# Optimization experiments

Hardware: AMD Instinct MI355X
Metric: run time of the kernel (lower is better)

Reference implementation:

```python
import jax, jax.numpy as jnp
import numpy as np

B = 4             # graphs per batch
POS_RANGE = 240.0 # pos lives in [0, 240)^3
VOXELS = (20.0, 30.0, 50.0, 80.0)
NEG = -1e30


def _basis(u):
    # open B-spline basis, degree 1, kernel_size 2, dim 3 -> 8 weights per edge
    cols = []
    for k in range(8):
        w = (u[:, 0] if k & 4 else 1.0 - u[:, 0])
        w = w * (u[:, 1] if k & 2 else 1.0 - u[:, 1])
        w = w * (u[:, 2] if k & 1 else 1.0 - u[:, 2])
        cols.append(w)
    return jnp.stack(cols, axis=1)  # [E, 8]


def _cartesian(pos, src, dst, emask):
    # T.Cartesian(cat=False, norm=True): rel pos scaled into [0,1]
    rel = pos[src] - pos[dst]
    m = jnp.max(jnp.where(emask[:, None], jnp.abs(rel), 0.0))
    return rel / (2.0 * jnp.maximum(m, 1e-9)) + 0.5


def _spline_conv(x, src, dst, pseudo, emask, W, Wr, b, n_nodes):
    # out_i = mean_{j->i} sum_k B_k(u_ij) x_j W_k + x_i Wr + b
    basis = _basis(pseudo) * emask[:, None].astype(x.dtype)  # [E,8]
    xk = jnp.einsum('ni,kio->nko', x, W)                     # [N,8,O]
    msg = basis[:, 0, None] * xk[src, 0]
    for k in range(1, 8):
        msg = msg + basis[:, k, None] * xk[src, k]           # [E,O]
    agg = jax.ops.segment_sum(msg, dst, num_segments=n_nodes)
    deg = jax.ops.segment_sum(emask.astype(x.dtype), dst, num_segments=n_nodes)
    return agg / jnp.maximum(deg, 1.0)[:, None] + x @ Wr + b


def _voxel_ids(pos, batch, vs):
    G = int(np.ceil(POS_RANGE / vs))
    c = jnp.clip(jnp.floor(pos / vs).astype(jnp.int64), 0, G - 1)
    cell = (c[:, 0] * G + c[:, 1]) * G + c[:, 2]
    return batch * (G ** 3) + cell, G ** 3


def _max_pool(x, pos, batch, valid, src, dst, emask, vs):
    # voxel-grid max pooling: nodes become fixed voxel cells (empty cells masked)
    nid, ncells = _voxel_ids(pos, batch, vs)
    n_new = B * ncells
    xm = jnp.where(valid[:, None], x, NEG)
    x_p = jax.ops.segment_max(xm, nid, num_segments=n_new)
    cnt = jax.ops.segment_sum(valid.astype(x.dtype), nid, num_segments=n_new)
    v_new = cnt > 0
    x_p = jnp.where(v_new[:, None], x_p, 0.0)
    pos_p = jax.ops.segment_sum(pos * valid[:, None].astype(pos.dtype), nid, num_segments=n_new)
    pos_p = pos_p / jnp.maximum(cnt, 1.0)[:, None]
    batch_p = jnp.arange(n_new, dtype=jnp.int64) // ncells
    # coarsen edges: remap to cells, drop self loops, coalesce at fixed size
    s2, d2 = nid[src], nid[dst]
    sent = n_new * n_new
    key = jnp.where(emask & (s2 != d2), s2 * n_new + d2, sent)
    uk = jnp.unique(key, size=key.shape[0], fill_value=sent)
    em = uk != sent
    uk = jnp.where(em, uk, 0)
    return x_p, pos_p, batch_p, v_new, uk // n_new, uk % n_new, em


def setup_inputs():
    key = jax.random.key(0)
    ks = jax.random.split(key, 24)
    NP, DEG = 5000, 8
    N = B * NP
    E = N * DEG
    x = jax.random.normal(ks[0], (N, 1), dtype=jnp.float32)
    pos = jax.random.uniform(ks[1], (N, 3), dtype=jnp.float32) * POS_RANGE
    src = jnp.repeat(jnp.arange(N, dtype=jnp.int64), DEG)
    delta = jax.random.randint(ks[2], (E,), 1, 100, dtype=jnp.int64)
    dst = (src // NP) * NP + (src % NP + delta) % NP   # intra-graph edges
    edge_index = jnp.stack([src, dst])
    batch = jnp.arange(N, dtype=jnp.int64) // NP
    sizes = [1, 64, 128, 256, 512]
    params = {}
    for l in range(4):
        ci, co = sizes[l], sizes[l + 1]
        params[f'W{l+1}'] = jax.random.normal(ks[3 + 3 * l], (8, ci, co), dtype=jnp.float32) / np.sqrt(8.0 * ci)
        params[f'Wr{l+1}'] = jax.random.normal(ks[4 + 3 * l], (ci, co), dtype=jnp.float32) / np.sqrt(float(ci))
        params[f'b{l+1}'] = jnp.zeros((co,), dtype=jnp.float32)
    params['fc1_w'] = jax.random.normal(ks[16], (64 * 512, 1024), dtype=jnp.float32) / np.sqrt(64.0 * 512.0)
    params['fc1_b'] = jnp.zeros((1024,), dtype=jnp.float32)
    params['fc2_w'] = jax.random.normal(ks[17], (1024, 1), dtype=jnp.float32) / np.sqrt(1024.0)
    params['fc2_b'] = jnp.zeros((1,), dtype=jnp.float32)
    return dict(x=x, pos=pos, edge_index=edge_index, batch=batch, **params)


def reference(x, pos, edge_index, batch, W1, Wr1, b1, W2, Wr2, b2, W3, Wr3, b3,
              W4, Wr4, b4, fc1_w, fc1_b, fc2_w, fc2_b):
    src, dst = edge_index[0], edge_index[1]
    n_nodes = x.shape[0]
    valid = jnp.ones((n_nodes,), dtype=bool)
    emask = jnp.ones((src.shape[0],), dtype=bool)
    Ws = [(W1, Wr1, b1), (W2, Wr2, b2), (W3, Wr3, b3), (W4, Wr4, b4)]
    for l in range(4):
        pseudo = _cartesian(pos, src, dst, emask)
        W, Wr, b = Ws[l]
        x = jax.nn.elu(_spline_conv(x, src, dst, pseudo, emask, W, Wr, b, n_nodes))
        if l < 3:
            x, pos, batch, valid, src, dst, emask = _max_pool(x, pos, batch, valid, src, dst, emask, VOXELS[l])
            n_nodes = x.shape[0]
    # MaxPoolingX(voxel=80, size=64): ceil(240/80)^3 = 27 <= 64 slots per graph
    nid, ncells = _voxel_ids(pos, batch, VOXELS[3])
    cluster = batch * 64 + (nid % ncells)
    xm = jnp.where(valid[:, None], x, NEG)
    xg = jax.ops.segment_max(xm, cluster, num_segments=B * 64)
    xg = jnp.where(xg <= NEG / 2, 0.0, xg)      # empty slots -> 0 (scatter-max default)
    xg = xg.reshape(B, 64 * 512)
    h = jax.nn.elu(xg @ fc1_w + fc1_b)           # dropout = identity (eval mode)
    return jax.nn.elu(h @ fc2_w + fc2_b)         # [B, 1]
```

## Files before the change

### kernel.cpp

```cpp
#include <hip/hip_runtime.h>

static constexpr int E0 = 160000;
static constexpr int NL0 = 20000;
static constexpr int NL1 = 6912;
static constexpr int NL2 = 2048;
static constexpr int NL3 = 500;

typedef short bf16x8 __attribute__((ext_vector_type(8)));
typedef float f32x4 __attribute__((ext_vector_type(4)));

__device__ __forceinline__ unsigned f2ord(float f) {
  unsigned u = __float_as_uint(f);
  return (u & 0x80000000u) ? ~u : (u | 0x80000000u);
}
__device__ __forceinline__ float ord2f(unsigned u) {
  unsigned v = (u & 0x80000000u) ? (u & 0x7fffffffu) : ~u;
  return __uint_as_float(v);
}
__device__ __forceinline__ float eluf(float x) { return x > 0.f ? x : expm1f(x); }
__device__ __forceinline__ void basis8(float u0, float u1, float u2, float* w) {
  float a0 = 1.f - u0, a1 = 1.f - u1, a2 = 1.f - u2;
  w[0] = a0*a1*a2; w[1] = a0*a1*u2; w[2] = a0*u1*a2; w[3] = a0*u1*u2;
  w[4] = u0*a1*a2; w[5] = u0*a1*u2; w[6] = u0*u1*a2; w[7] = u0*u1*u2;
}
__device__ __forceinline__ unsigned short f2b(float f) {
  unsigned u = __float_as_uint(f);
  return (unsigned short)((u + 0x7fffu + ((u >> 16) & 1u)) >> 16);
}
__device__ __forceinline__ float b2f(unsigned short h) {
  return __uint_as_float(((unsigned)h) << 16);
}
__device__ __forceinline__ int clampi(int v, int lo, int hi) {
  return v < lo ? lo : (v > hi ? hi : v);
}

__device__ __forceinline__ void mfma_tile(const unsigned short* __restrict__ Ah,
    const unsigned short* __restrict__ Al, const unsigned short* __restrict__ Bh,
    const unsigned short* __restrict__ Bl, int M, long K, int m0, int n0,
    int kbeg, int ksl, char* smem, f32x4* acc) {
  auto Ash = (unsigned short (*)[40])(smem);
  auto Asl = (unsigned short (*)[40])(smem + 5120);
  auto Bsh = (unsigned short (*)[40])(smem + 10240);
  auto Bsl = (unsigned short (*)[40])(smem + 15360);
  int t = threadIdx.x;
  int r = t >> 2, sg = (t & 3) * 8;
  int w = t >> 6, lane = t & 63;
  int ar = (w << 4) + (lane & 15), kq = (lane >> 4) << 3;
  for (int kt = 0; kt < ksl; kt += 32) {
    bf16x8 va = {}, vl = {};
    if (m0 + r < M) {
      long ga = (long)(m0 + r) * K + kbeg + kt + sg;
      va = *(const bf16x8*)&Ah[ga];
      vl = *(const bf16x8*)&Al[ga];
    }
    *(bf16x8*)&Ash[r][sg] = va;
    *(bf16x8*)&Asl[r][sg] = vl;
    long gb = (long)(n0 + r) * K + kbeg + kt + sg;
    *(bf16x8*)&Bsh[r][sg] = *(const bf16x8*)&Bh[gb];
    *(bf16x8*)&Bsl[r][sg] = *(const bf16x8*)&Bl[gb];
    __syncthreads();
    bf16x8 ah = *(const bf16x8*)&Ash[ar][kq];
    bf16x8 al = *(const bf16x8*)&Asl[ar][kq];
    #pragma unroll
    for (int nt = 0; nt < 4; nt++) {
      int br = (nt << 4) + (lane & 15);
      bf16x8 bh = *(const bf16x8*)&Bsh[br][kq];
      bf16x8 bl = *(const bf16x8*)&Bsl[br][kq];
      acc[nt] = __builtin_amdgcn_mfma_f32_16x16x32_bf16(al, bh, acc[nt], 0, 0, 0);
      acc[nt] = __builtin_amdgcn_mfma_f32_16x16x32_bf16(ah, bl, acc[nt], 0, 0, 0);
      acc[nt] = __builtin_amdgcn_mfma_f32_16x16x32_bf16(ah, bh, acc[nt], 0, 0, 0);
    }
    __syncthreads();
  }
}

__global__ __launch_bounds__(256)
void k_prep(const int* __restrict__ src0, const int* __restrict__ dst0,
            const float* __restrict__ pos0, const float* __restrict__ x0,
            int* __restrict__ degi, int4* __restrict__ erec0u, float* __restrict__ mbuf,
            unsigned* __restrict__ zA, long zAw,
            const float* __restrict__ W1, const float* __restrict__ Wr1, float* __restrict__ wc1,
            const float* __restrict__ W2, const float* __restrict__ Wr2,
            const float* __restrict__ W3, const float* __restrict__ Wr3,
            const float* __restrict__ W4, const float* __restrict__ Wr4,
            unsigned short* __restrict__ w2h, unsigned short* __restrict__ w2l,
            unsigned short* __restrict__ w3h, unsigned short* __restrict__ w3l,
            unsigned short* __restrict__ w4h, unsigned short* __restrict__ w4l) {
  __shared__ __align__(16) float T[64][65];
  __shared__ float red[4];
  int tid = blockIdx.x * 256 + threadIdx.x;
  long gsz = (long)gridDim.x * 256;
  for (long i = tid; i < zAw; i += gsz) zA[i] = 0u;
  float v = 0.f;
  for (int e = tid; e < E0; e += (int)gsz) {
    int s = src0[e], d = dst0[e];
    atomicAdd(&degi[d], 1);
    float r0 = pos0[s*3]   - pos0[d*3];
    float r1 = pos0[s*3+1] - pos0[d*3+1];
    float r2 = pos0[s*3+2] - pos0[d*3+2];
    erec0u[e] = make_int4(__float_as_int(x0[s]), __float_as_int(r0),
                          __float_as_int(r1), __float_as_int(r2));
    v = fmaxf(v, fmaxf(fabsf(r0), fmaxf(fabsf(r1), fabsf(r2))));
  }
  #pragma unroll
  for (int off = 32; off; off >>= 1) v = fmaxf(v, __shfl_down(v, off, 64));
  if ((threadIdx.x & 63) == 0) red[threadIdx.x >> 6] = v;
  __syncthreads();
  if (threadIdx.x == 0)
    atomicMax((unsigned*)mbuf,
              __float_as_uint(fmaxf(fmaxf(red[0], red[1]), fmaxf(red[2], red[3]))));
  for (int b = blockIdx.x; b < 378; b += gridDim.x) {
    const float *W, *Wr; unsigned short *oh, *ol; int K, N, kt, nt;
    if (b < 18)      { W = W2; Wr = Wr2; oh = w2h; ol = w2l; K = 576;  N = 128; kt = b / 2; nt = b % 2; }
    else if (b < 90) { int q = b - 18; W = W3; Wr = Wr3; oh = w3h; ol = w3l; K = 1152; N = 256; kt = q / 4; nt = q % 4; }
    else             { int q = b - 90; W = W4; Wr = Wr4; oh = w4h; ol = w4l; K = 2304; N = 512; kt = q / 8; nt = q % 8; }
    int k0 = kt * 64, n0 = nt * 64, KW = K - K / 9;
    __syncthreads();
    for (int i = threadIdx.x; i < 4096; i += 256) {
      int kk = i >> 6, nn = i & 63, k = k0 + kk;
      T[kk][nn] = (k < KW) ? W[(long)k * N + n0 + nn] : Wr[(long)(k - KW) * N + n0 + nn];
    }
    __syncthreads();
    for (int i = threadIdx.x; i < 4096; i += 256) {
      int nn = i >> 6, kk = i & 63;
      float vv = T[kk][nn];
      unsigned short hu = f2b(vv), lu = f2b(vv - b2f(hu));
      long o = (long)(n0 + nn) * K + k0 + kk;
      oh[o] = hu; ol[o] = lu;
    }
  }
  if (blockIdx.x == 0)
    for (int i = threadIdx.x; i < 576; i += 256)
      wc1[i] = (i < 512) ? W1[i] : Wr1[i - 512];
}

__global__ void k_alloc(int* __restrict__ degi, int* __restrict__ rowbeg,
                        int* __restrict__ rowlen, int* __restrict__ cursor,
                        int* __restrict__ ctr, int N) {
  int n = blockIdx.x * 256 + threadIdx.x;
  if (n >= N) return;
  int len = degi[n];
  int st = atomicAdd(ctr, len);
  rowbeg[n] = st; cursor[n] = st; rowlen[n] = len; degi[n] = 0;
}

__global__ void k_scat(const int4* __restrict__ eu, const int* __restrict__ du,
                       const int* __restrict__ ecnt, int ecap,
                       int* __restrict__ cursor, int4* __restrict__ es) {
  int n = ecnt ? *ecnt : ecap;
  for (int e = blockIdx.x * 256 + threadIdx.x; e < n; e += gridDim.x * 256) {
    int p = atomicAdd(&cursor[du[e]], 1);
    es[p] = eu[e];
  }
}

__global__ __launch_bounds__(256)
void k_l1(const int4* __restrict__ erec, const int* __restrict__ rowbeg,
          const int* __restrict__ rowlen, const float* __restrict__ mbuf,
          const float* __restrict__ x0, const float* __restrict__ pos0,
          const float* __restrict__ wc1, const float* __restrict__ b1,
          unsigned* __restrict__ pord1, float* __restrict__ cnt1,
          float* __restrict__ possum1, int* __restrict__ nid) {
  __shared__ float wls[576];
  __shared__ float b1s[64];
  __shared__ float ys[32][12];
  int t = threadIdx.x;
  for (int i = t; i < 576; i += 256) wls[i] = wc1[i];
  if (t < 64) b1s[t] = b1[t];
  int d = blockIdx.x * 32 + (t >> 3);
  int sub = t & 7;
  float inv = 0.5f / fmaxf(mbuf[0], 1e-9f);
  if (d < NL0) {
    int beg = rowbeg[d], len = rowlen[d], end = beg + len;
    float acc[8] = {};
    for (int j = beg + sub; j < end; j += 8) {
      int4 rc = erec[j];
      float xv = __int_as_float(rc.x);
      float w[8];
      basis8(__int_as_float(rc.y) * inv + 0.5f, __int_as_float(rc.z) * inv + 0.5f,
             __int_as_float(rc.w) * inv + 0.5f, w);
      #pragma unroll
      for (int k = 0; k < 8; k++) acc[k] += w[k] * xv;
    }
    #pragma unroll
    for (int m = 1; m < 8; m <<= 1)
      #pragma unroll
      for (int k = 0; k < 8; k++) acc[k] += __shfl_xor(acc[k], m, 64);
    if (sub == 0) {
      float sc = 1.f / fmaxf((float)len, 1.f);
      int nl = t >> 3;
      #pragma unroll
      for (int k = 0; k < 8; k++) ys[nl][k] = acc[k] * sc;
      ys[nl][8]  = x0[d];
      ys[nl][9]  = pos0[d*3];
      ys[nl][10] = pos0[d*3+1];
      ys[nl][11] = pos0[d*3+2];
    }
  }
  __syncthreads();
  #pragma unroll 2
  for (int it = 0; it < 8; it++) {
    int idx = it * 256 + t;
    int nl = idx >> 6, ch = idx & 63;
    int dd = blockIdx.x * 32 + nl;
    if (dd < NL0) {
      float v = b1s[ch] + ys[nl][8] * wls[512 + ch];
      #pragma unroll
      for (int k = 0; k < 8; k++) v += ys[nl][k] * wls[k * 64 + ch];
      v = eluf(v);
      float pd0 = ys[nl][9], pd1 = ys[nl][10], pd2 = ys[nl][11];
      int c0 = clampi((int)floorf(pd0 / 20.f), 0, 11);
      int c1 = clampi((int)floorf(pd1 / 20.f), 0, 11);
      int c2 = clampi((int)floorf(pd2 / 20.f), 0, 11);
      int id = (dd / 5000) * 1728 + (c0 * 12 + c1) * 12 + c2;
      atomicMax(&pord1[(long)id * 64 + ch], f2ord(v));
      if (ch == 0) {
        nid[dd] = id;
        atomicAdd(&cnt1[id], 1.f);
        atomicAdd(&possum1[id*3],   pd0);
        atomicAdd(&possum1[id*3+1], pd1);
        atomicAdd(&possum1[id*3+2], pd2);
      }
    }
  }
}

__global__ __launch_bounds__(256)
void k_pedge(const int4* __restrict__ erecf, const int* __restrict__ srcf,
             const int* __restrict__ dstf, const int* __restrict__ ecntf, int ecap,
             const int* __restrict__ nid, int Nn, unsigned* __restrict__ bitmap,
             int4* __restrict__ erecu, int* __restrict__ dstu, int* __restrict__ ecntc,
             int* __restrict__ degi, const float* __restrict__ possum,
             const float* __restrict__ cnt, float* __restrict__ mo) {
  __shared__ float red[4];
  int n = ecntf ? *ecntf : ecap;
  int lane = threadIdx.x & 63;
  int stride = gridDim.x * 256;
  float vmax = 0.f;
  for (int base = blockIdx.x * 256; base < n; base += stride) {
    int e = base + threadIdx.x;
    bool win = false;
    int s2 = 0, d2 = 0;
    float r0 = 0.f, r1 = 0.f, r2 = 0.f;
    if (e < n) {
      int sL = erecf ? erecf[e].x : srcf[e];
      int dL = dstf[e];
      s2 = nid[sL]; d2 = nid[dL];
      if (s2 != d2) {
        float ics = 1.f / fmaxf(cnt[s2], 1.f), icd = 1.f / fmaxf(cnt[d2], 1.f);
        r0 = possum[s2*3]   * ics - possum[d2*3]   * icd;
        r1 = possum[s2*3+1] * ics - possum[d2*3+1] * icd;
        r2 = possum[s2*3+2] * ics - possum[d2*3+2] * icd;
        vmax = fmaxf(vmax, fmaxf(fabsf(r0), fmaxf(fabsf(r1), fabsf(r2))));
        unsigned key = (unsigned)s2 * (unsigned)Nn + (unsigned)d2;
        unsigned bit = 1u << (key & 31);
        unsigned old = atomicOr(&bitmap[key >> 5], bit);
        win = !(old & bit);
      }
    }
    unsigned long long mask = __ballot(win);
    if (mask) {
      int leader = __ffsll((unsigned long long)mask) - 1;
      int bq = 0;
      if (lane == leader) bq = atomicAdd(ecntc, __popcll(mask));
      bq = __shfl(bq, leader, 64);
      if (win) {
        int q = bq + __popcll(mask & ((1ULL << lane) - 1ULL));
        erecu[q] = make_int4(s2, __float_as_int(r0), __float_as_int(r1), __float_as_int(r2));
        dstu[q] = d2;
        atomicAdd(&degi[d2], 1);
      }
    }
  }
  #pragma unroll
  for (int off = 32; off; off >>= 1) vmax = fmaxf(vmax, __shfl_down(vmax, off, 64));
  if ((threadIdx.x & 63) == 0) red[threadIdx.x >> 6] = vmax;
  __syncthreads();
  if (threadIdx.x == 0)
    atomicMax((unsigned*)mo,
              __float_as_uint(fmaxf(fmaxf(red[0], red[1]), fmaxf(red[2], red[3]))));
}

template<int ES>
__global__ __launch_bounds__(256)
void k_gather(const unsigned* __restrict__ pordc, const int4* __restrict__ erec,
              const int* __restrict__ rowbeg, const int* __restrict__ rowlen,
              const float* __restrict__ mbuf,
              unsigned short* __restrict__ ysh, unsigned short* __restrict__ ysl,
              int N, int Ci, int nchunk,
              unsigned* __restrict__ zp, long zw) {
  for (long i = (long)blockIdx.x * 256 + threadIdx.x; i < zw;
       i += (long)gridDim.x * 256) zp[i] = 0u;
  __shared__ float comb[4][64][8];
  int wv = threadIdx.x >> 6, lane = threadIdx.x & 63;
  int gw = blockIdx.x * 4 + wv;
  int job = gw / ES, sub = gw % ES;
  int d = job / nchunk, ch = job % nchunk;
  bool active = d < N;
  float inv = 0.5f / fmaxf(mbuf[0], 1e-9f);
  int co = ch * 64 + lane;
  float acc[8] = {};
  int beg = 0, len = 0;
  if (active) {
    beg = rowbeg[d]; len = rowlen[d];
    int end = beg + len;
    int j = beg + sub;
    for (; j + 3 * ES < end; j += 4 * ES) {
      int4 ra = erec[j], rb = erec[j + ES], rc = erec[j + 2 * ES], rd = erec[j + 3 * ES];
      float xa = ord2f(pordc[(long)ra.x * Ci + co]);
      float xb = ord2f(pordc[(long)rb.x * Ci + co]);
      float xc = ord2f(pordc[(long)rc.x * Ci + co]);
      float xd = ord2f(pordc[(long)rd.x * Ci + co]);
      float wa[8], wb[8], wc[8], wd[8];
      basis8(__int_as_float(ra.y) * inv + 0.5f, __int_as_float(ra.z) * inv + 0.5f,
             __int_as_float(ra.w) * inv + 0.5f, wa);
      basis8(__int_as_float(rb.y) * inv + 0.5f, __int_as_float(rb.z) * inv + 0.5f,
             __int_as_float(rb.w) * inv + 0.5f, wb);
      basis8(__int_as_float(rc.y) * inv + 0.5f, __int_as_float(rc.z) * inv + 0.5f,
             __int_as_float(rc.w) * inv + 0.5f, wc);
      basis8(__int_as_float(rd.y) * inv + 0.5f, __int_as_float(rd.z) * inv + 0.5f,
             __int_as_float(rd.w) * inv + 0.5f, wd);
      #pragma unroll
      for (int k = 0; k < 8; k++)
        acc[k] += wa[k] * xa + wb[k] * xb + wc[k] * xc + wd[k] * xd;
    }
    for (; j < end; j += ES) {
      int4 ra = erec[j];
      float xa = ord2f(pordc[(long)ra.x * Ci + co]);
      float wa[8];
      basis8(__int_as_float(ra.y) * inv + 0.5f, __int_as_float(ra.z) * inv + 0.5f,
             __int_as_float(ra.w) * inv + 0.5f, wa);
      #pragma unroll
      for (int k = 0; k < 8; k++) acc[k] += wa[k] * xa;
    }
  }
  if (ES > 1) {
    #pragma unroll
    for (int k = 0; k < 8; k++) comb[wv][lane][k] = acc[k];
    __syncthreads();
    if (sub != 0 || !active) return;
    #pragma unroll
    for (int s = 1; s < ES; s++)
      #pragma unroll
      for (int k = 0; k < 8; k++) acc[k] += comb[wv + s][lane][k];
  } else if (!active) return;
  float sc = 1.f / fmaxf((float)len, 1.f);
  long row = (long)d * 9 * Ci;
  #pragma unroll
  for (int k = 0; k < 8; k++) {
    float v = acc[k] * sc;
    unsigned short hu = f2b(v);
    ysh[row + k * Ci + co] = hu;
    ysl[row + k * Ci + co] = f2b(v - b2f(hu));
  }
  unsigned od = pordc[(long)d * Ci + co];
  float xdv = (od == 0u) ? 0.f : ord2f(od);
  unsigned short hu = f2b(xdv);
  ysh[row + 8 * Ci + co] = hu;
  ysl[row + 8 * Ci + co] = f2b(xdv - b2f(hu));
}

__global__ __launch_bounds__(256)
void k_gemmpool(const unsigned short* __restrict__ ysh, const unsigned short* __restrict__ ysl,
                const unsigned short* __restrict__ Bh, const unsigned short* __restrict__ Bl,
                int M, int N, int K, const float* __restrict__ bias,
                const float* __restrict__ possum, const float* __restrict__ cnt,
                int div, float vs, int G, int NC,
                unsigned* __restrict__ pordn, float* __restrict__ cntn,
                float* __restrict__ possumn, int* __restrict__ nid) {
  __shared__ __align__(16) char smem[20480];
  int nbx = N >> 6;
  int bx = blockIdx.x % nbx, by = blockIdx.x / nbx;
  int m0 = by * 64, n0 = bx * 64;
  f32x4 acc[4] = {};
  mfma_tile(ysh, ysl, Bh, Bl, M, K, m0, n0, 0, K, smem, acc);
  int w = threadIdx.x >> 6, lane = threadIdx.x & 63;
  int row0 = m0 + (w << 4) + ((lane >> 4) << 2);
  int colb = n0 + (lane & 15);
  #pragma unroll
  for (int q = 0; q < 4; q++) {
    int gm = row0 + q;
    float c = cnt[gm];
    float ic = 1.f / fmaxf(c, 1.f);
    float p0 = possum[gm*3] * ic, p1 = possum[gm*3+1] * ic, p2 = possum[gm*3+2] * ic;
    int c0 = clampi((int)floorf(p0 / vs), 0, G - 1);
    int c1 = clampi((int)floorf(p1 / vs), 0, G - 1);
    int c2 = clampi((int)floorf(p2 / vs), 0, G - 1);
    int id = (gm / div) * NC + (c0 * G + c1) * G + c2;
    bool vl = c > 0.f;
    if (bx == 0 && (lane & 15) == 0) {
      nid[gm] = id;
      if (vl) {
        atomicAdd(&cntn[id], 1.f);
        atomicAdd(&possumn[id*3],   p0);
        atomicAdd(&possumn[id*3+1], p1);
        atomicAdd(&possumn[id*3+2], p2);
      }
    }
    if (vl) {
      #pragma unroll
      for (int nt = 0; nt < 4; nt++) {
        int col = colb + nt * 16;
        float v = eluf(acc[nt][q] + bias[col]);
        atomicMax(&pordn[(long)id * N + col], f2ord(v));
      }
    }
  }
}

__global__ __launch_bounds__(256)
void k_gemm4(const unsigned short* __restrict__ ysh, const unsigned short* __restrict__ ysl,
             const unsigned short* __restrict__ Bh, const unsigned short* __restrict__ Bl,
             float* __restrict__ Cp, int* __restrict__ done,
             const float* __restrict__ b4, const float* __restrict__ possum3,
             const float* __restrict__ cnt3, unsigned* __restrict__ xg) {
  __shared__ __align__(16) char smem[20480];
  __shared__ int flag;
  int z = blockIdx.x >> 6, rem = blockIdx.x & 63, bx = rem & 7, by = rem >> 3;
  int m0 = by * 64, n0 = bx * 64;
  f32x4 acc[4] = {};
  mfma_tile(ysh, ysl, Bh, Bl, 500, 2304, m0, n0, z * 576, 576, smem, acc);
  float* Co = Cp + (long)z * 256000;
  int w = threadIdx.x >> 6, lane = threadIdx.x & 63;
  int row0 = m0 + (w << 4) + ((lane >> 4) << 2);
  int colb = n0 + (lane & 15);
  #pragma unroll
  for (int nt = 0; nt < 4; nt++)
    #pragma unroll
    for (int q = 0; q < 4; q++) {
      int gm = row0 + q;
      if (gm < 500) Co[(long)gm * 512 + colb + nt * 16] = acc[nt][q];
    }
  __threadfence();
  if (threadIdx.x == 0) flag = atomicAdd(&done[rem], 1);
  __syncthreads();
  if (flag != 3) return;
  __threadfence();
  #pragma unroll
  for (int q = 0; q < 4; q++) {
    int gm = row0 + q;
    if (gm >= 500) continue;
    float c = cnt3[gm];
    if (c <= 0.f) continue;
    float ic = 1.f / c;
    float p0 = possum3[gm*3] * ic, p1 = possum3[gm*3+1] * ic, p2 = possum3[gm*3+2] * ic;
    int c0 = clampi((int)floorf(p0 / 80.f), 0, 2);
    int c1 = clampi((int)floorf(p1 / 80.f), 0, 2);
    int c2 = clampi((int)floorf(p2 / 80.f), 0, 2);
    int cl = (gm / 125) * 64 + (c0 * 3 + c1) * 3 + c2;
    #pragma unroll
    for (int nt = 0; nt < 4; nt++) {
      int col = colb + nt * 16;
      long idx = (long)gm * 512 + col;
      float s = Cp[idx] + Cp[idx + 256000] + Cp[idx + 512000] + Cp[idx + 768000];
      float v = eluf(s + b4[col]);
      atomicMax(&xg[(long)cl * 512 + col], f2ord(v));
    }
  }
}

__global__ __launch_bounds__(128)
void k_fc1(const unsigned* __restrict__ xg_ord, const float* __restrict__ w,
           float* __restrict__ h) {
  int cellhalf = blockIdx.x >> 4;
  int r = blockIdx.x & 15;
  int jb = r >> 1, ciq = r & 1;
  int cell = cellhalf >> 1, half = cellhalf & 1;
  int j = jb * 128 + threadIdx.x;
  __shared__ float xs[4][128];
  for (int q = threadIdx.x; q < 512; q += 128) {
    int b = q >> 7, ci = q & 127;
    unsigned o = xg_ord[((b * 64 + cell) << 9) + half * 256 + ciq * 128 + ci];
    xs[b][ci] = (o == 0u) ? 0.f : ord2f(o);
  }
  __syncthreads();
  float a0 = 0, a1 = 0, a2 = 0, a3 = 0;
  int cbase = cell * 512 + half * 256 + ciq * 128;
  #pragma unroll 2
  for (int ci = 0; ci < 128; ci++) {
    float ww = w[(long)(cbase + ci) * 1024 + j];
    a0 += xs[0][ci] * ww; a1 += xs[1][ci] * ww;
    a2 += xs[2][ci] * ww; a3 += xs[3][ci] * ww;
  }
  atomicAdd(&h[j], a0);        atomicAdd(&h[1024 + j], a1);
  atomicAdd(&h[2048 + j], a2); atomicAdd(&h[3072 + j], a3);
}

__global__ void k_fc2(const float* __restrict__ h, const float* __restrict__ fb1,
                      const float* __restrict__ w, const float* __restrict__ b,
                      float* __restrict__ out) {
  int bb = blockIdx.x, t = threadIdx.x;
  float a = 0;
  for (int j = t; j < 1024; j += 256) a += eluf(h[bb * 1024 + j] + fb1[j]) * w[j];
  for (int off = 32; off; off >>= 1) a += __shfl_down(a, off, 64);
  __shared__ float red[4];
  int lane = t & 63, wv = t >> 6;
  if (lane == 0) red[wv] = a;
  __syncthreads();
  if (t == 0) out[bb] = eluf(red[0] + red[1] + red[2] + red[3] + b[0]);
}

extern "C" void kernel_launch(void* const* d_in, const int* in_sizes, int n_in,
                              void* d_out, int out_size, void* d_ws, size_t ws_size,
                              hipStream_t stream) {
  const float* x0   = (const float*)d_in[0];
  const float* pos0 = (const float*)d_in[1];
  const int*   ei   = (const int*)d_in[2];
  const float* W1 = (const float*)d_in[4],  *Wr1 = (const float*)d_in[5],  *b1 = (const float*)d_in[6];
  const float* W2 = (const float*)d_in[7],  *Wr2 = (const float*)d_in[8],  *b2 = (const float*)d_in[9];
  const float* W3 = (const float*)d_in[10], *Wr3 = (const float*)d_in[11], *b3 = (const float*)d_in[12];
  const float* W4 = (const float*)d_in[13], *Wr4 = (const float*)d_in[14], *b4 = (const float*)d_in[15];
  const float* fw1 = (const float*)d_in[16], *fb1 = (const float*)d_in[17];
  const float* fw2 = (const float*)d_in[18], *fb2 = (const float*)d_in[19];
  float* out = (float*)d_out;
  const int* src0 = ei;
  const int* dst0 = ei + E0;

  char* ws = (char*)d_ws;
  size_t off = 0;
  auto alloc = [&](size_t bytes) -> void* {
    off = (off + 255) & ~(size_t)255;
    void* q = ws + off; off += bytes; return q;
  };
  int4* erec0u = (int4*)alloc((size_t)E0 * 16);
  int4* erec_s = (int4*)alloc((size_t)E0 * 16);
  int4* eu_a   = (int4*)alloc((size_t)E0 * 16);
  int4* eu_b   = (int4*)alloc((size_t)E0 * 16);
  int* du_a = (int*)alloc(E0 * 4);
  int* du_b = (int*)alloc(E0 * 4);
  int* nid  = (int*)alloc(NL0 * 4);
  int* rowbeg = (int*)alloc(NL0 * 4);
  int* rowlen = (int*)alloc(NL0 * 4);
  int* cursor = (int*)alloc(NL0 * 4);
  unsigned short* ysh = (unsigned short*)alloc((size_t)NL1 * 576 * 2);
  unsigned short* ysl = (unsigned short*)alloc((size_t)NL1 * 576 * 2);
  float* wc1 = (float*)alloc(576 * 4);
  unsigned short* w2h = (unsigned short*)alloc((size_t)576 * 128 * 2);
  unsigned short* w2l = (unsigned short*)alloc((size_t)576 * 128 * 2);
  unsigned short* w3h = (unsigned short*)alloc((size_t)1152 * 256 * 2);
  unsigned short* w3l = (unsigned short*)alloc((size_t)1152 * 256 * 2);
  unsigned short* w4h = (unsigned short*)alloc((size_t)2304 * 512 * 2);
  unsigned short* w4l = (unsigned short*)alloc((size_t)2304 * 512 * 2);
  float* Cp = (float*)alloc((size_t)4 * 256000 * 4);
  char* tz = (char*)alloc(0);
  float* mbuf = (float*)alloc(32);
  int* ecnt = (int*)alloc(32);
  int* ctr  = (int*)alloc(32);
  int* done = (int*)alloc(64 * 4);
  int* degi = (int*)alloc(NL0 * 4);
  float* h  = (float*)alloc(4096 * 4);
  char* tzend = (char*)alloc(0);
  size_t tzbytes = (size_t)(tzend - tz);
  char* zA = (char*)alloc(0);
  size_t bm1w = ((size_t)NL1 * NL1 + 31) / 32;
  unsigned* bm1 = (unsigned*)alloc(bm1w * 4);
  unsigned* pord1 = (unsigned*)alloc((size_t)NL1 * 64 * 4);
  float* cnt1 = (float*)alloc(NL1 * 4);
  float* possum1 = (float*)alloc(NL1 * 12);
  char* zAend = (char*)alloc(0);
  long zAw = (long)(zAend - zA) / 4;
  char* zB = (char*)alloc(0);
  size_t bm2w = ((size_t)NL2 * NL2 + 31) / 32;
  unsigned* bm2 = (unsigned*)alloc(bm2w * 4);
  unsigned* pord2 = (unsigned*)alloc((size_t)NL2 * 128 * 4);
  float* cnt2 = (float*)alloc(NL2 * 4);
  float* possum2 = (float*)alloc(NL2 * 12);
  char* zBend = (char*)alloc(0);
  long zBw = (long)(zBend - zB) / 4;
  char* zC = (char*)alloc(0);
  size_t bm3w = ((size_t)NL3 * NL3 + 31) / 32;
  unsigned* bm3 = (unsigned*)alloc(bm3w * 4);
  unsigned* pord3 = (unsigned*)alloc((size_t)NL3 * 256 * 4);
  float* cnt3 = (float*)alloc(NL3 * 4);
  float* possum3 = (float*)alloc(NL3 * 12);
  char* zCend = (char*)alloc(0);
  long zCw = (long)(zCend - zC) / 4;
  unsigned* xg = (unsigned*)alloc((size_t)4 * 64 * 512 * 4);
  long zDw = 4 * 64 * 512;
  (void)ws_size; (void)in_sizes; (void)n_in; (void)out_size;

  auto cdiv = [](long a, long b) { return (int)((a + b - 1) / b); };

  hipMemsetAsync(tz, 0, tzbytes, stream);

  k_prep<<<512, 256, 0, stream>>>(src0, dst0, pos0, x0, degi, erec0u, mbuf, (unsigned*)zA, zAw,
                                  W1, Wr1, wc1, W2, Wr2, W3, Wr3, W4, Wr4,
                                  w2h, w2l, w3h, w3l, w4h, w4l);
  k_alloc<<<cdiv(NL0, 256), 256, 0, stream>>>(degi, rowbeg, rowlen, cursor, ctr + 0, NL0);
  k_scat<<<512, 256, 0, stream>>>(erec0u, dst0, nullptr, E0, cursor, erec_s);
  k_l1<<<cdiv(NL0, 32), 256, 0, stream>>>(erec_s, rowbeg, rowlen, mbuf, x0, pos0,
                                          wc1, b1, pord1, cnt1, possum1, nid);
  k_pedge<<<512, 256, 0, stream>>>(nullptr, src0, dst0, nullptr, E0, nid, NL1, bm1,
                                   eu_a, du_a, ecnt + 0, degi, possum1, cnt1, mbuf + 1);
  k_alloc<<<cdiv(NL1, 256), 256, 0, stream>>>(degi, rowbeg, rowlen, cursor, ctr + 1, NL1);
  k_scat<<<512, 256, 0, stream>>>(eu_a, du_a, ecnt + 0, E0, cursor, erec_s);
  k_gather<2><<<cdiv((long)NL1 * 2, 4), 256, 0, stream>>>(pord1, erec_s, rowbeg, rowlen, mbuf + 1,
                                                          ysh, ysl, NL1, 64, 1, (unsigned*)zB, zBw);
  k_gemmpool<<<(128 / 64) * (NL1 / 64), 256, 0, stream>>>(
      ysh, ysl, w2h, w2l, NL1, 128, 576, b2, possum1, cnt1,
      1728, 30.f, 8, 512, pord2, cnt2, possum2, nid);
  k_pedge<<<512, 256, 0, stream>>>(eu_a, nullptr, du_a, ecnt + 0, E0, nid, NL2, bm2,
                                   eu_b, du_b, ecnt + 1, degi, possum2, cnt2, mbuf + 2);
  k_alloc<<<cdiv(NL2, 256), 256, 0, stream>>>(degi, rowbeg, rowlen, cursor, ctr + 2, NL2);
  k_scat<<<512, 256, 0, stream>>>(eu_b, du_b, ecnt + 1, E0, cursor, erec_s);
  k_gather<4><<<cdiv((long)NL2 * 2 * 4, 4), 256, 0, stream>>>(pord2, erec_s, rowbeg, rowlen, mbuf + 2,
                                                              ysh, ysl, NL2, 128, 2, (unsigned*)zC, zCw);
  k_gemmpool<<<(256 / 64) * (NL2 / 64), 256, 0, stream>>>(
      ysh, ysl, w3h, w3l, NL2, 256, 1152, b3, possum2, cnt2,
      512, 50.f, 5, 125, pord3, cnt3, possum3, nid);
  k_pedge<<<512, 256, 0, stream>>>(eu_b, nullptr, du_b, ecnt + 1, E0, nid, NL3, bm3,
                                   eu_a, du_a, ecnt + 2, degi, possum3, cnt3, mbuf + 3);
  k_alloc<<<cdiv(NL3, 256), 256, 0, stream>>>(degi, rowbeg, rowlen, cursor, ctr + 3, NL3);
  k_scat<<<512, 256, 0, stream>>>(eu_a, du_a, ecnt + 2, E0, cursor, erec_s);
  k_gather<4><<<cdiv((long)NL3 * 4 * 4, 4), 256, 0, stream>>>(pord3, erec_s, rowbeg, rowlen, mbuf + 3,
                                                              ysh, ysl, NL3, 256, 4, xg, zDw);
  k_gemm4<<<256, 256, 0, stream>>>(ysh, ysl, w4h, w4l, Cp, done, b4, possum3, cnt3, xg);
  k_fc1<<<27 * 2 * 8 * 2, 128, 0, stream>>>(xg, fw1, h);
  k_fc2<<<4, 256, 0, stream>>>(h, fb1, fw2, fb2, out);
}
```

Before: 417.7 us.

## Split layer-1 kernel, add split-K to pooled GEMMs, fuse fc2 into fc1

Layer 1 is split into an edge-aggregation kernel that writes per-node basis sums to a global buffer, and a separate per-node kernel that does the 9x64 projection, ELU and voxel pooling. This removes the shared-memory staging and the block-wide barrier. The layer-2 and layer-3 GEMM+pool kernels now use split-K: partial tiles go to a scratch buffer and the last-arriving block of each tile sums them and runs the pooling epilogue. Gather template widths are reduced, and fc2 is folded into fc1 through a last-block-done counter, which removes one launch. These changes add scratch-memory traffic, atomic counters and serial tail work in exchange for more parallelism and fewer launches.

```diff
diff --git a/kernel.cpp b/kernel.cpp
--- a/kernel.cpp
+++ b/kernel.cpp
@@ -155,73 +155,69 @@
 }
 
 __global__ __launch_bounds__(256)
-void k_l1(const int4* __restrict__ erec, const int* __restrict__ rowbeg,
-          const int* __restrict__ rowlen, const float* __restrict__ mbuf,
-          const float* __restrict__ x0, const float* __restrict__ pos0,
-          const float* __restrict__ wc1, const float* __restrict__ b1,
-          unsigned* __restrict__ pord1, float* __restrict__ cnt1,
-          float* __restrict__ possum1, int* __restrict__ nid) {
-  __shared__ float wls[576];
-  __shared__ float b1s[64];
-  __shared__ float ys[32][12];
+void k_l1a(const int4* __restrict__ erec, const int* __restrict__ rowbeg,
+           const int* __restrict__ rowlen, const float* __restrict__ mbuf,
+           float* __restrict__ ysg) {
   int t = threadIdx.x;
-  for (int i = t; i < 576; i += 256) wls[i] = wc1[i];
-  if (t < 64) b1s[t] = b1[t];
   int d = blockIdx.x * 32 + (t >> 3);
+  if (d >= NL0) return;
   int sub = t & 7;
   float inv = 0.5f / fmaxf(mbuf[0], 1e-9f);
-  if (d < NL0) {
-    int beg = rowbeg[d], len = rowlen[d], end = beg + len;
-    float acc[8] = {};
-    for (int j = beg + sub; j < end; j += 8) {
-      int4 rc = erec[j];
-      float xv = __int_as_float(rc.x);
-      float w[8];
-      basis8(__int_as_float(rc.y) * inv + 0.5f, __int_as_float(rc.z) * inv + 0.5f,
-             __int_as_float(rc.w) * inv + 0.5f, w);
-      #pragma unroll
-      for (int k = 0; k < 8; k++) acc[k] += w[k] * xv;
-    }
-    #pragma unroll
-    for (int m = 1; m < 8; m <<= 1)
-      #pragma unroll
-      for (int k = 0; k < 8; k++) acc[k] += __shfl_xor(acc[k], m, 64);
-    if (sub == 0) {
-      float sc = 1.f / fmaxf((float)len, 1.f);
-      int nl = t >> 3;
-      #pragma unroll
-      for (int k = 0; k < 8; k++) ys[nl][k] = acc[k] * sc;
-      ys[nl][8]  = x0[d];
-      ys[nl][9]  = pos0[d*3];
-      ys[nl][10] = pos0[d*3+1];
-      ys[nl][11] = pos0[d*3+2];
-    }
-  }
-  __syncthreads();
-  #pragma unroll 2
-  for (int it = 0; it < 8; it++) {
-    int idx = it * 256 + t;
-    int nl = idx >> 6, ch = idx & 63;
-    int dd = blockIdx.x * 32 + nl;
-    if (dd < NL0) {
-      float v = b1s[ch] + ys[nl][8] * wls[512 + ch];
-      #pragma unroll
-      for (int k = 0; k < 8; k++) v += ys[nl][k] * wls[k * 64 + ch];
-      v = eluf(v);
-      float pd0 = ys[nl][9], pd1 = ys[nl][10], pd2 = ys[nl][11];
-      int c0 = clampi((int)floorf(pd0 / 20.f), 0, 11);
-      int c1 = clampi((int)floorf(pd1 / 20.f), 0, 11);
-      int c2 = clampi((int)floorf(pd2 / 20.f), 0, 11);
-      int id = (dd / 5000) * 1728 + (c0 * 12 + c1) * 12 + c2;
-      atomicMax(&pord1[(long)id * 64 + ch], f2ord(v));
-      if (ch == 0) {
-        nid[dd] = id;
-        atomicAdd(&cnt1[id], 1.f);
-        atomicAdd(&possum1[id*3],   pd0);
-        atomicAdd(&possum1[id*3+1], pd1);
-        atomicAdd(&possum1[id*3+2], pd2);
-      }
-    }
+  int beg = rowbeg[d], len = rowlen[d], end = beg + len;
+  float acc[8] = {};
+  for (int j = beg + sub; j < end; j += 8) {
+    int4 rc = erec[j];
+    float xv = __int_as_float(rc.x);
+    float w[8];
+    basis8(__int_as_float(rc.y) * inv + 0.5f, __int_as_float(rc.z) * inv + 0.5f,
+           __int_as_float(rc.w) * inv + 0.5f, w);
+    #pragma unroll
+    for (int k = 0; k < 8; k++) acc[k] += w[k] * xv;
+  }
+  #pragma unroll
+  for (int m = 1; m < 8; m <<= 1)
+    #pragma unroll
+    for (int k = 0; k < 8; k++) acc[k] += __shfl_xor(acc[k], m, 64);
+  if (sub == 0) {
+    float sc = 1.f / fmaxf((float)len, 1.f);
+    float4 o0 = make_float4(acc[0]*sc, acc[1]*sc, acc[2]*sc, acc[3]*sc);
+    float4 o1 = make_float4(acc[4]*sc, acc[5]*sc, acc[6]*sc, acc[7]*sc);
+    *(float4*)&ysg[d*8]     = o0;
+    *(float4*)&ysg[d*8 + 4] = o1;
+  }
+}
+
+__global__ __launch_bounds__(256)
+void k_l1b(const float* __restrict__ ysg, const float* __restrict__ x0,
+           const float* __restrict__ pos0, const float* __restrict__ wc1,
+           const float* __restrict__ b1,
+           unsigned* __restrict__ pord1, float* __restrict__ cnt1,
+           float* __restrict__ possum1, int* __restrict__ nid) {
+  int wv = threadIdx.x >> 6, lane = threadIdx.x & 63;
+  int d = blockIdx.x * 4 + wv;
+  if (d >= NL0) return;
+  float wcol[9];
+  #pragma unroll
+  for (int k = 0; k < 8; k++) wcol[k] = wc1[k * 64 + lane];
+  wcol[8] = wc1[512 + lane];
+  float4 a0 = *(const float4*)&ysg[d*8];
+  float4 a1 = *(const float4*)&ysg[d*8 + 4];
+  float v = b1[lane] + x0[d] * wcol[8]
+          + a0.x * wcol[0] + a0.y * wcol[1] + a0.z * wcol[2] + a0.w * wcol[3]
+          + a1.x * wcol[4] + a1.y * wcol[5] + a1.z * wcol[6] + a1.w * wcol[7];
+  v = eluf(v);
+  float pd0 = pos0[d*3], pd1 = pos0[d*3+1], pd2 = pos0[d*3+2];
+  int c0 = clampi((int)floorf(pd0 / 20.f), 0, 11);
+  int c1 = clampi((int)floorf(pd1 / 20.f), 0, 11);
+  int c2 = clampi((int)floorf(pd2 / 20.f), 0, 11);
+  int id = (d / 5000) * 1728 + (c0 * 12 + c1) * 12 + c2;
+  atomicMax(&pord1[(long)id * 64 + lane], f2ord(v));
+  if (lane == 0) {
+    nid[d] = id;
+    atomicAdd(&cnt1[id], 1.f);
+    atomicAdd(&possum1[id*3],   pd0);
+    atomicAdd(&possum1[id*3+1], pd1);
+    atomicAdd(&possum1[id*3+2], pd2);
   }
 }
 
@@ -363,20 +359,36 @@
 __global__ __launch_bounds__(256)
 void k_gemmpool(const unsigned short* __restrict__ ysh, const unsigned short* __restrict__ ysl,
                 const unsigned short* __restrict__ Bh, const unsigned short* __restrict__ Bl,
-                int M, int N, int K, const float* __restrict__ bias,
+                int M, int N, int K, int ntile, const float* __restrict__ bias,
                 const float* __restrict__ possum, const float* __restrict__ cnt,
                 int div, float vs, int G, int NC,
                 unsigned* __restrict__ pordn, float* __restrict__ cntn,
-                float* __restrict__ possumn, int* __restrict__ nid) {
+                float* __restrict__ possumn, int* __restrict__ nid,
+                float* __restrict__ Cp, int* __restrict__ done_t) {
   __shared__ __align__(16) char smem[20480];
+  __shared__ int flag;
+  int zc = gridDim.x / ntile;
+  int tile = blockIdx.x % ntile, zid = blockIdx.x / ntile;
   int nbx = N >> 6;
-  int bx = blockIdx.x % nbx, by = blockIdx.x / nbx;
+  int bx = tile % nbx, by = tile / nbx;
   int m0 = by * 64, n0 = bx * 64;
+  int ksl = K / zc;
   f32x4 acc[4] = {};
-  mfma_tile(ysh, ysl, Bh, Bl, M, K, m0, n0, 0, K, smem, acc);
+  mfma_tile(ysh, ysl, Bh, Bl, M, K, m0, n0, zid * ksl, ksl, smem, acc);
   int w = threadIdx.x >> 6, lane = threadIdx.x & 63;
   int row0 = m0 + (w << 4) + ((lane >> 4) << 2);
   int colb = n0 + (lane & 15);
+  float* Co = Cp + (long)zid * M * N;
+  #pragma unroll
+  for (int nt = 0; nt < 4; nt++)
+    #pragma unroll
+    for (int q = 0; q < 4; q++)
+      Co[(long)(row0 + q) * N + colb + nt * 16] = acc[nt][q];
+  __threadfence();
+  if (threadIdx.x == 0) flag = atomicAdd(&done_t[tile], 1);
+  __syncthreads();
+  if (flag != zc - 1) return;
+  __threadfence();
   #pragma unroll
   for (int q = 0; q < 4; q++) {
     int gm = row0 + q;
@@ -401,7 +413,10 @@
       #pragma unroll
       for (int nt = 0; nt < 4; nt++) {
         int col = colb + nt * 16;
-        float v = eluf(acc[nt][q] + bias[col]);
+        long idx = (long)gm * N + col;
+        float s = 0.f;
+        for (int zz = 0; zz < zc; zz++) s += Cp[(long)zz * M * N + idx];
+        float v = eluf(s + bias[col]);
         atomicMax(&pordn[(long)id * N + col], f2ord(v));
       }
     }
@@ -461,43 +476,46 @@
 
 __global__ __launch_bounds__(128)
 void k_fc1(const unsigned* __restrict__ xg_ord, const float* __restrict__ w,
-           float* __restrict__ h) {
-  int cellhalf = blockIdx.x >> 4;
-  int r = blockIdx.x & 15;
-  int jb = r >> 1, ciq = r & 1;
+           float* __restrict__ h, int* __restrict__ donef,
+           const float* __restrict__ fb1, const float* __restrict__ fw2,
+           const float* __restrict__ fb2, float* __restrict__ out) {
+  int cellhalf = blockIdx.x >> 3, jb = blockIdx.x & 7;
   int cell = cellhalf >> 1, half = cellhalf & 1;
   int j = jb * 128 + threadIdx.x;
-  __shared__ float xs[4][128];
-  for (int q = threadIdx.x; q < 512; q += 128) {
-    int b = q >> 7, ci = q & 127;
-    unsigned o = xg_ord[((b * 64 + cell) << 9) + half * 256 + ciq * 128 + ci];
+  __shared__ float xs[4][256];
+  __shared__ int flg;
+  __shared__ float red2[2];
+  for (int q = threadIdx.x; q < 1024; q += 128) {
+    int b = q >> 8, ci = q & 255;
+    unsigned o = xg_ord[((b * 64 + cell) << 9) + half * 256 + ci];
     xs[b][ci] = (o == 0u) ? 0.f : ord2f(o);
   }
   __syncthreads();
   float a0 = 0, a1 = 0, a2 = 0, a3 = 0;
-  int cbase = cell * 512 + half * 256 + ciq * 128;
-  #pragma unroll 2
-  for (int ci = 0; ci < 128; ci++) {
+  int cbase = cell * 512 + half * 256;
+  for (int ci = 0; ci < 256; ci++) {
     float ww = w[(long)(cbase + ci) * 1024 + j];
     a0 += xs[0][ci] * ww; a1 += xs[1][ci] * ww;
     a2 += xs[2][ci] * ww; a3 += xs[3][ci] * ww;
   }
   atomicAdd(&h[j], a0);        atomicAdd(&h[1024 + j], a1);
   atomicAdd(&h[2048 + j], a2); atomicAdd(&h[3072 + j], a3);
-}
-
-__global__ void k_fc2(const float* __restrict__ h, const float* __restrict__ fb1,
-                      const float* __restrict__ w, const float* __restrict__ b,
-                      float* __restrict__ out) {
-  int bb = blockIdx.x, t = threadIdx.x;
-  float a = 0;
-  for (int j = t; j < 1024; j += 256) a += eluf(h[bb * 1024 + j] + fb1[j]) * w[j];
-  for (int off = 32; off; off >>= 1) a += __shfl_down(a, off, 64);
-  __shared__ float red[4];
-  int lane = t & 63, wv = t >> 6;
-  if (lane == 0) red[wv] = a;
+  __threadfence();
+  if (threadIdx.x == 0) flg = atomicAdd(donef, 1);
   __syncthreads();
-  if (t == 0) out[bb] = eluf(red[0] + red[1] + red[2] + red[3] + b[0]);
+  if (flg != 431) return;
+  __threadfence();
+  for (int bb = 0; bb < 4; bb++) {
+    float a = 0.f;
+    for (int j2 = threadIdx.x; j2 < 1024; j2 += 128)
+      a += eluf(h[bb * 1024 + j2] + fb1[j2]) * fw2[j2];
+    #pragma unroll
+    for (int off2 = 32; off2; off2 >>= 1) a += __shfl_down(a, off2, 64);
+    if ((threadIdx.x & 63) == 0) red2[threadIdx.x >> 6] = a;
+    __syncthreads();
+    if (threadIdx.x == 0) out[bb] = eluf(red2[0] + red2[1] + fb2[0]);
+    __syncthreads();
+  }
 }
 
 extern "C" void kernel_launch(void* const* d_in, const int* in_sizes, int n_in,
@@ -532,6 +550,7 @@
   int* rowbeg = (int*)alloc(NL0 * 4);
   int* rowlen = (int*)alloc(NL0 * 4);
   int* cursor = (int*)alloc(NL0 * 4);
+  float* ysg = (float*)alloc((size_t)NL0 * 8 * 4);
   unsigned short* ysh = (unsigned short*)alloc((size_t)NL1 * 576 * 2);
   unsigned short* ysl = (unsigned short*)alloc((size_t)NL1 * 576 * 2);
   float* wc1 = (float*)alloc(576 * 4);
@@ -541,12 +560,12 @@
   unsigned short* w3l = (unsigned short*)alloc((size_t)1152 * 256 * 2);
   unsigned short* w4h = (unsigned short*)alloc((size_t)2304 * 512 * 2);
   unsigned short* w4l = (unsigned short*)alloc((size_t)2304 * 512 * 2);
-  float* Cp = (float*)alloc((size_t)4 * 256000 * 4);
+  float* Cp = (float*)alloc((size_t)4 * 6912 * 128 * 4);
   char* tz = (char*)alloc(0);
   float* mbuf = (float*)alloc(32);
   int* ecnt = (int*)alloc(32);
   int* ctr  = (int*)alloc(32);
-  int* done = (int*)alloc(64 * 4);
+  int* done = (int*)alloc(1024 * 4);
   int* degi = (int*)alloc(NL0 * 4);
   float* h  = (float*)alloc(4096 * 4);
   char* tzend = (char*)alloc(0);
@@ -588,33 +607,32 @@
                                   w2h, w2l, w3h, w3l, w4h, w4l);
   k_alloc<<<cdiv(NL0, 256), 256, 0, stream>>>(degi, rowbeg, rowlen, cursor, ctr + 0, NL0);
   k_scat<<<512, 256, 0, stream>>>(erec0u, dst0, nullptr, E0, cursor, erec_s);
-  k_l1<<<cdiv(NL0, 32), 256, 0, stream>>>(erec_s, rowbeg, rowlen, mbuf, x0, pos0,
-                                          wc1, b1, pord1, cnt1, possum1, nid);
+  k_l1a<<<cdiv(NL0, 32), 256, 0, stream>>>(erec_s, rowbeg, rowlen, mbuf, ysg);
+  k_l1b<<<cdiv(NL0, 4), 256, 0, stream>>>(ysg, x0, pos0, wc1, b1, pord1, cnt1, possum1, nid);
   k_pedge<<<512, 256, 0, stream>>>(nullptr, src0, dst0, nullptr, E0, nid, NL1, bm1,
                                    eu_a, du_a, ecnt + 0, degi, possum1, cnt1, mbuf + 1);
   k_alloc<<<cdiv(NL1, 256), 256, 0, stream>>>(degi, rowbeg, rowlen, cursor, ctr + 1, NL1);
   k_scat<<<512, 256, 0, stream>>>(eu_a, du_a, ecnt + 0, E0, cursor, erec_s);
-  k_gather<2><<<cdiv((long)NL1 * 2, 4), 256, 0, stream>>>(pord1, erec_s, rowbeg, rowlen, mbuf + 1,
-                                                          ysh, ysl, NL1, 64, 1, (unsigned*)zB, zBw);
-  k_gemmpool<<<(128 / 64) * (NL1 / 64), 256, 0, stream>>>(
-      ysh, ysl, w2h, w2l, NL1, 128, 576, b2, possum1, cnt1,
-      1728, 30.f, 8, 512, pord2, cnt2, possum2, nid);
+  k_gather<1><<<cdiv(NL1, 4), 256, 0, stream>>>(pord1, erec_s, rowbeg, rowlen, mbuf + 1,
+                                                ysh, ysl, NL1, 64, 1, (unsigned*)zB, zBw);
+  k_gemmpool<<<3 * 2 * (NL1 / 64), 256, 0, stream>>>(
+      ysh, ysl, w2h, w2l, NL1, 128, 576, 2 * (NL1 / 64), b2, possum1, cnt1,
+      1728, 30.f, 8, 512, pord2, cnt2, possum2, nid, Cp, done + 0);
   k_pedge<<<512, 256, 0, stream>>>(eu_a, nullptr, du_a, ecnt + 0, E0, nid, NL2, bm2,
                                    eu_b, du_b, ecnt + 1, degi, possum2, cnt2, mbuf + 2);
   k_alloc<<<cdiv(NL2, 256), 256, 0, stream>>>(degi, rowbeg, rowlen, cursor, ctr + 2, NL2);
   k_scat<<<512, 256, 0, stream>>>(eu_b, du_b, ecnt + 1, E0, cursor, erec_s);
-  k_gather<4><<<cdiv((long)NL2 * 2 * 4, 4), 256, 0, stream>>>(pord2, erec_s, rowbeg, rowlen, mbuf + 2,
+  k_gather<2><<<cdiv((long)NL2 * 2 * 2, 4), 256, 0, stream>>>(pord2, erec_s, rowbeg, rowlen, mbuf + 2,
                                                               ysh, ysl, NL2, 128, 2, (unsigned*)zC, zCw);
-  k_gemmpool<<<(256 / 64) * (NL2 / 64), 256, 0, stream>>>(
-      ysh, ysl, w3h, w3l, NL2, 256, 1152, b3, possum2, cnt2,
-      512, 50.f, 5, 125, pord3, cnt3, possum3, nid);
+  k_gemmpool<<<4 * 4 * (NL2 / 64), 256, 0, stream>>>(
+      ysh, ysl, w3h, w3l, NL2, 256, 1152, 4 * (NL2 / 64), b3, possum2, cnt2,
+      512, 50.f, 5, 125, pord3, cnt3, possum3, nid, Cp, done + 256);
   k_pedge<<<512, 256, 0, stream>>>(eu_b, nullptr, du_b, ecnt + 1, E0, nid, NL3, bm3,
                                    eu_a, du_a, ecnt + 2, degi, possum3, cnt3, mbuf + 3);
   k_alloc<<<cdiv(NL3, 256), 256, 0, stream>>>(degi, rowbeg, rowlen, cursor, ctr + 3, NL3);
   k_scat<<<512, 256, 0, stream>>>(eu_a, du_a, ecnt + 2, E0, cursor, erec_s);
   k_gather<4><<<cdiv((long)NL3 * 4 * 4, 4), 256, 0, stream>>>(pord3, erec_s, rowbeg, rowlen, mbuf + 3,
                                                               ysh, ysl, NL3, 256, 4, xg, zDw);
-  k_gemm4<<<256, 256, 0, stream>>>(ysh, ysl, w4h, w4l, Cp, done, b4, possum3, cnt3, xg);
-  k_fc1<<<27 * 2 * 8 * 2, 128, 0, stream>>>(xg, fw1, h);
-  k_fc2<<<4, 256, 0, stream>>>(h, fb1, fw2, fb2, out);
-}
+  k_gemm4<<<256, 256, 0, stream>>>(ysh, ysl, w4h, w4l, Cp, done + 512, b4, possum3, cnt3, xg);
+  k_fc1<<<27 * 2 * 8, 128, 0, stream>>>(xg, fw1, h, done + 768, fb1, fw2, fb2, out);
+}
```

Measured after the change: 624.8 us. 49.6% more time.
